# Optimization experiments

Measured on AMD Instinct MI355X. Metric: run time of the kernel, lower is better.

The kernel has to match this reference:

```python
import jax, jax.numpy as jnp
import numpy as np
from jax import lax

B, T, I, H, O = 256, 128, 512, 1024, 512


def setup_inputs() -> dict:
    key = jax.random.key(0)
    ks = jax.random.split(key, 7)
    s = 1.0 / np.sqrt(H)  # PyTorch LSTM/Linear init bound
    x = jax.random.normal(ks[0], (B, T, I), dtype=jnp.float32)
    W_ih = jax.random.uniform(ks[1], (4 * H, I), jnp.float32, -s, s)
    W_hh = jax.random.uniform(ks[2], (4 * H, H), jnp.float32, -s, s)
    b_ih = jax.random.uniform(ks[3], (4 * H,), jnp.float32, -s, s)
    b_hh = jax.random.uniform(ks[4], (4 * H,), jnp.float32, -s, s)
    W_fc = jax.random.uniform(ks[5], (O, H), jnp.float32, -s, s)
    b_fc = jax.random.uniform(ks[6], (O,), jnp.float32, -s, s)
    return {"x": x, "W_ih": W_ih, "W_hh": W_hh, "b_ih": b_ih,
            "b_hh": b_hh, "W_fc": W_fc, "b_fc": b_fc}


def _lstm_last(x, W_ih, W_hh, b_ih, b_hh):
    # Precompute input contribution for all timesteps: [T, B, 4H]
    pre = jnp.einsum('bti,gi->tbg', x, W_ih) + b_ih + b_hh

    def step(carry, xg):
        h, c = carry
        gates = xg + h @ W_hh.T  # [B, 4H]
        i, f, g, o = jnp.split(gates, 4, axis=-1)  # PyTorch gate order i,f,g,o
        c = jax.nn.sigmoid(f) * c + jax.nn.sigmoid(i) * jnp.tanh(g)
        h = jax.nn.sigmoid(o) * jnp.tanh(c)
        return (h, c), None

    h0 = jnp.zeros((x.shape[0], W_hh.shape[1]), x.dtype)
    (h, c), _ = lax.scan(step, (h0, h0), pre)
    return h, c


def reference(x, W_ih, W_hh, b_ih, b_hh, W_fc, b_fc):
    h, c = _lstm_last(x, W_ih, W_hh, b_ih, b_hh)
    out = h @ W_fc.T + b_fc  # fc on last timestep hidden
    # hidden returned as (h_n, c_n) with leading n_layers=1 dim, as in PyTorch
    return out, (h[None], c[None])
```

## Files before the change

kernel.cpp:

```cpp
#include <hip/hip_runtime.h>

typedef short bf8 __attribute__((ext_vector_type(8)));
typedef float f32x4 __attribute__((ext_vector_type(4)));
typedef uint u32x4 __attribute__((ext_vector_type(4)));

static constexpr int BB = 256;
static constexpr int TT = 128;
static constexpr int II = 512;
static constexpr int HH = 1024;
static constexpr int OO = 512;
static constexpr int G4 = 4096;

static constexpr size_t OUT_H = (size_t)BB * OO;
static constexpr size_t OUT_C = OUT_H + (size_t)BB * HH;
static constexpr size_t HBUF  = (size_t)BB * HH;

__device__ __forceinline__ float bf2f(ushort u) {
    unsigned v = ((unsigned)u) << 16;
    return __builtin_bit_cast(float, v);
}
__device__ __forceinline__ ushort f2bf(float f) {
    unsigned x = __builtin_bit_cast(unsigned, f);
    x = x + 0x7FFFu + ((x >> 16) & 1u);
    return (ushort)(x >> 16);
}
__device__ __forceinline__ float sigf(float x) { return 1.0f / (1.0f + __expf(-x)); }
__device__ __forceinline__ float tanhf_(float x) { return 2.0f * sigf(2.0f * x) - 1.0f; }

__device__ __forceinline__ void st_wt_short(const ushort* p, uint v) {
    asm volatile("global_store_short %0, %1, off sc0 sc1" :: "v"(p), "v"(v) : "memory");
}
__device__ __forceinline__ void st_wt_b64(const ushort* p, uint2 v) {
    asm volatile("global_store_dwordx2 %0, %1, off sc0 sc1" :: "v"(p), "v"(v) : "memory");
}
__device__ __forceinline__ void ld_bp_ushort_issue(uint& dst, const ushort* p) {
    asm volatile("global_load_ushort %0, %1, off sc0 sc1" : "=v"(dst) : "v"(p) : "memory");
}
__device__ __forceinline__ void ld_bp_b128_issue(u32x4& dst, const ushort* p) {
    asm volatile("global_load_dwordx4 %0, %1, off sc0 sc1" : "=v"(dst) : "v"(p) : "memory");
}
__device__ __forceinline__ void ld_c_b128_issue(u32x4& dst, const ushort* p) {
    asm volatile("global_load_dwordx4 %0, %1, off" : "=v"(dst) : "v"(p) : "memory");
}
__device__ __forceinline__ void wait_vm0() {
    asm volatile("s_waitcnt vmcnt(0)" ::: "memory");
    __builtin_amdgcn_sched_barrier(0);
}
#define WAITVM(N) do { asm volatile("s_waitcnt vmcnt(" #N ")" ::: "memory"); \
                       __builtin_amdgcn_sched_barrier(0); } while (0)

__device__ __forceinline__ void lightbar(int* slots, int bg, int gen) {
    asm volatile("s_waitcnt vmcnt(0) lgkmcnt(0)" ::: "memory");
    __builtin_amdgcn_sched_barrier(0);
    __syncthreads();
    int tid = threadIdx.x;
    if (tid == 0)
        asm volatile("global_store_dword %0, %1, off sc0 sc1" :: "v"(slots + bg * 32), "v"(gen) : "memory");
    if (tid < 64) {
        const int* sp = slots + tid * 32;
        int v;
        do {
            asm volatile("global_load_dword %0, %1, off sc0 sc1\n\ts_waitcnt vmcnt(0)"
                         : "=v"(v) : "v"(sp) : "memory");
            if (v >= gen) break;
            __builtin_amdgcn_s_sleep(1);
        } while (true);
    }
    __syncthreads();
}

__global__ void k_init(int* flags) {
    int i = blockIdx.x * 256 + threadIdx.x;
    if (i < 8192) flags[i] = 0;
}

__global__ void k_cast(const float* __restrict__ src, ushort* __restrict__ dst, int n4) {
    int i = blockIdx.x * blockDim.x + threadIdx.x;
    int stride = gridDim.x * blockDim.x;
    for (; i < n4; i += stride) {
        float4 v = ((const float4*)src)[i];
        ushort4 o;
        o.x = f2bf(v.x); o.y = f2bf(v.y); o.z = f2bf(v.z); o.w = f2bf(v.w);
        ((ushort4*)dst)[i] = o;
    }
}

__global__ void k_prep_w(const float* __restrict__ w, ushort* __restrict__ wp,
                         const float* __restrict__ bi, const float* __restrict__ bh,
                         float* __restrict__ bp, int Kdim) {
    int p = blockIdx.x;
    int orig = ((p >> 4) & 3) * HH + ((p >> 6) << 4) + (p & 15);
    const float* src = w + (size_t)orig * Kdim;
    ushort* dst = wp + (size_t)p * Kdim;
    for (int k = threadIdx.x; k < Kdim; k += 256) dst[k] = f2bf(src[k]);
    if (threadIdx.x == 0 && bp) bp[p] = bi[orig] + bh[orig];
}

template <int HMODE>
__global__ __launch_bounds__(256) void k_main(
    const float* __restrict__ x, const ushort* __restrict__ wpih,
    const float* __restrict__ bp, ushort* __restrict__ pre,
    const ushort* __restrict__ wphh, ushort* __restrict__ hbf,
    float* __restrict__ dout, int* flags, int SEG) {
    __shared__ ushort wl[32 * 2048];
    __shared__ ushort Al[64 * 32];
    __shared__ ushort Bl[128 * 32];

    int tid = threadIdx.x;
    int bid = blockIdx.x;
    int g = bid >> 6, j = bid & 63;
    int row0 = g << 6;
    int* slots = flags + g * 2048;
    int gen = 0;
    int nseg = TT / SEG;

    int w = tid >> 6, l = tid & 63;
    int l15 = l & 15, kg = l >> 4;
    int wbase = ((l15 << 6) + (kg << 4)) ^ ((l15 & 7) << 4);

    {
        const ushort* wsrc = wphh + (size_t)(j << 6) * HH;
        for (int s = 0; s < 32; ++s) {
            int cidx = (s << 8) + tid;
            int c = cidx >> 7;
            int kc = cidx & 127;
            uint4 v = *(const uint4*)(wsrc + (size_t)c * HH + (kc << 3));
            int byte = ((kc >> 2) << 12) + ((((c << 6) + ((kc & 3) << 4))) ^ ((c & 7) << 4));
            *(uint4*)((char*)wl + byte) = v;
        }
        int r = tid >> 2, hc = (tid & 3) << 2;
        uint2 z; z.x = 0; z.y = 0;
        st_wt_b64(hbf + (size_t)(row0 + r) * HH + (j << 4) + hc, z);
    }

    int wm = w >> 1, wn = w & 1;
    int r0 = tid >> 2, kk = tid & 3;
    int sbyteA = ((r0 << 6) + (kk << 4)) ^ ((r0 & 7) << 4);
    int sbyteB1 = sbyteA + 4096;

    const ushort* hbase = hbf + (size_t)(row0 + (w << 4) + l15) * HH + (kg << 3);
    int drow = row0 + (w << 4) + (kg << 2);
    int hcol = (j << 4) + l15;
    ushort* hobase = hbf + (size_t)drow * HH + hcol;
    const ushort* pbase = pre + (size_t)drow * G4 + (j << 6) + l15;
    float creg[4] = {0.f, 0.f, 0.f, 0.f};

    for (int sg = 0; sg < nseg; ++sg) {
        int t0 = sg * SEG;
        int ntiles = SEG << 5;
        for (int q = j; q < ntiles; q += 64) {
            int trel = q >> 5;
            int t = t0 + trel;
            int n0 = (q & 31) << 7;
            const float* xa = x + ((size_t)(row0 + r0) * TT + t) * II + (kk << 3);
            const ushort* gb0 = wpih + (size_t)(n0 + r0) * II + (kk << 3);
            const ushort* gb1 = gb0 + (size_t)64 * II;
            f32x4 acc[2][4];
#pragma unroll
            for (int mi = 0; mi < 2; ++mi)
#pragma unroll
                for (int ni = 0; ni < 4; ++ni) acc[mi][ni] = f32x4{0.f, 0.f, 0.f, 0.f};
            float4 a0 = *(const float4*)xa;
            float4 a1 = *(const float4*)(xa + 4);
            uint4 b0v = *(const uint4*)gb0;
            uint4 b1v = *(const uint4*)gb1;
            for (int ko = 0; ko < 16; ++ko) {
                union { ushort us[8]; uint4 v; } pa;
                pa.us[0] = f2bf(a0.x); pa.us[1] = f2bf(a0.y); pa.us[2] = f2bf(a0.z); pa.us[3] = f2bf(a0.w);
                pa.us[4] = f2bf(a1.x); pa.us[5] = f2bf(a1.y); pa.us[6] = f2bf(a1.z); pa.us[7] = f2bf(a1.w);
                __syncthreads();
                *(uint4*)((char*)Al + sbyteA) = pa.v;
                *(uint4*)((char*)Bl + sbyteA) = b0v;
                *(uint4*)((char*)Bl + sbyteB1) = b1v;
                __syncthreads();
                if (ko < 15) {
                    int k = (ko + 1) << 5;
                    a0 = *(const float4*)(xa + k);
                    a1 = *(const float4*)(xa + k + 4);
                    b0v = *(const uint4*)(gb0 + k);
                    b1v = *(const uint4*)(gb1 + k);
                }
                bf8 af[2], bv[4];
#pragma unroll
                for (int mi = 0; mi < 2; ++mi)
                    af[mi] = *(const bf8*)((char*)Al + wm * 2048 + mi * 1024 + wbase);
#pragma unroll
                for (int ni = 0; ni < 4; ++ni)
                    bv[ni] = *(const bf8*)((char*)Bl + wn * 4096 + ni * 1024 + wbase);
#pragma unroll
                for (int mi = 0; mi < 2; ++mi)
#pragma unroll
                    for (int ni = 0; ni < 4; ++ni)
                        acc[mi][ni] = __builtin_amdgcn_mfma_f32_16x16x32_bf16(af[mi], bv[ni], acc[mi][ni], 0, 0, 0);
            }
#pragma unroll
            for (int ni = 0; ni < 4; ++ni) {
                int col = n0 + wn * 64 + ni * 16 + l15;
                float bias = bp[col];
#pragma unroll
                for (int mi = 0; mi < 2; ++mi) {
                    int arow = row0 + wm * 32 + mi * 16 + (kg << 2);
#pragma unroll
                    for (int r = 0; r < 4; ++r)
                        st_wt_short(pre + ((size_t)trel * BB + arow + r) * G4 + col,
                                    (uint)f2bf(acc[mi][ni][r] + bias));
                }
            }
        }
        gen++; lightbar(slots, j, gen);

        uint prn[16];
#pragma unroll
        for (int ni = 0; ni < 4; ++ni)
#pragma unroll
            for (int r = 0; r < 4; ++r)
                ld_bp_ushort_issue(prn[ni * 4 + r], pbase + (size_t)r * G4 + (ni << 4));
        wait_vm0();

        for (int trel = 0; trel < SEG; ++trel) {
            int t = t0 + trel;
            int rb = HMODE ? (t & 1) : t;
            int wb = HMODE ? ((t & 1) ^ 1) : (t + 1);
            const ushort* hr = hbase + (size_t)rb * HBUF;
            u32x4 xv[8], yv[8];

#define ISSUE8(B, C) \
            _Pragma("unroll") \
            for (int u = 0; u < 8; ++u) { \
                if constexpr (HMODE == 0) ld_c_b128_issue(B[u], hr + (((C) * 8 + u) << 5)); \
                else ld_bp_b128_issue(B[u], hr + (((C) * 8 + u) << 5)); \
            }
#define CONSUME8(B, C) \
            _Pragma("unroll") \
            for (int u = 0; u < 8; ++u) { \
                int ko = (C) * 8 + u; \
                bf8 a = __builtin_bit_cast(bf8, B[u]); \
                _Pragma("unroll") \
                for (int ni = 0; ni < 4; ++ni) { \
                    bf8 b = *(const bf8*)((char*)wl + ko * 4096 + ni * 1024 + wbase); \
                    acc[ni] = __builtin_amdgcn_mfma_f32_16x16x32_bf16(a, b, acc[ni], 0, 0, 0); \
                } \
            }

            f32x4 acc[4];
            ISSUE8(xv, 0)
            ISSUE8(yv, 1)
#pragma unroll
            for (int ni = 0; ni < 4; ++ni)
#pragma unroll
                for (int r = 0; r < 4; ++r) acc[ni][r] = bf2f((ushort)prn[ni * 4 + r]);
            WAITVM(8);
            CONSUME8(xv, 0)
            ISSUE8(xv, 2)
            WAITVM(8);
            CONSUME8(yv, 1)
            ISSUE8(yv, 3)
            WAITVM(8);
            CONSUME8(xv, 2)
            {
                int nrel = (trel + 1 < SEG) ? trel + 1 : 0;
                const ushort* pnn = pre + ((size_t)nrel * BB + drow) * G4 + (j << 6) + l15;
#pragma unroll
                for (int ni = 0; ni < 4; ++ni)
#pragma unroll
                    for (int r = 0; r < 4; ++r)
                        ld_bp_ushort_issue(prn[ni * 4 + r], pnn + (size_t)r * G4 + (ni << 4));
            }
            WAITVM(16);
            CONSUME8(yv, 3)
#undef ISSUE8
#undef CONSUME8

            ushort* ho = hobase + (size_t)wb * HBUF;
            bool last = (t == TT - 1);
#pragma unroll
            for (int r = 0; r < 4; ++r) {
                float ig = sigf(acc[0][r]);
                float fg = sigf(acc[1][r]);
                float gg = tanhf_(acc[2][r]);
                float og = sigf(acc[3][r]);
                float c = fg * creg[r] + ig * gg;
                creg[r] = c;
                float h = og * tanhf_(c);
                st_wt_short(ho + (size_t)r * HH, (uint)f2bf(h));
                if (last) {
                    dout[OUT_H + (size_t)(drow + r) * HH + hcol] = h;
                    dout[OUT_C + (size_t)(drow + r) * HH + hcol] = c;
                }
            }
            gen++; lightbar(slots, j, gen);
        }
    }
}

__global__ __launch_bounds__(256) void k_fc(const ushort* __restrict__ hlast,
                                            const ushort* __restrict__ wfc,
                                            const float* __restrict__ bfc,
                                            float* __restrict__ out) {
    int tid = threadIdx.x;
    int b0 = (blockIdx.x >> 3) << 6;
    int n0 = (blockIdx.x & 7) << 6;
    int w = tid >> 6, l = tid & 63;
    int l15 = l & 15, kg = l >> 4;
    const ushort* ha = hlast + (size_t)(b0 + (w << 4) + l15) * HH + (kg << 3);
    f32x4 acc[4];
#pragma unroll
    for (int ni = 0; ni < 4; ++ni) acc[ni] = f32x4{0.f, 0.f, 0.f, 0.f};
    for (int ko = 0; ko < 32; ++ko) {
        bf8 a = *(const bf8*)(ha + (ko << 5));
#pragma unroll
        for (int ni = 0; ni < 4; ++ni) {
            bf8 b = *(const bf8*)(wfc + (size_t)(n0 + ni * 16 + l15) * HH + (ko << 5) + (kg << 3));
            acc[ni] = __builtin_amdgcn_mfma_f32_16x16x32_bf16(a, b, acc[ni], 0, 0, 0);
        }
    }
    int drow = b0 + (w << 4) + (kg << 2);
#pragma unroll
    for (int ni = 0; ni < 4; ++ni) {
        int col = n0 + ni * 16 + l15;
        float bias = bfc[col];
#pragma unroll
        for (int r = 0; r < 4; ++r)
            out[(size_t)(drow + r) * OO + col] = acc[ni][r] + bias;
    }
}

extern "C" void kernel_launch(void* const* d_in, const int* in_sizes, int n_in,
                              void* d_out, int out_size, void* d_ws, size_t ws_size,
                              hipStream_t stream) {
    const float* x   = (const float*)d_in[0];
    const float* Wih = (const float*)d_in[1];
    const float* Whh = (const float*)d_in[2];
    const float* bih = (const float*)d_in[3];
    const float* bhh = (const float*)d_in[4];
    const float* Wfc = (const float*)d_in[5];
    const float* bfc = (const float*)d_in[6];
    float* out = (float*)d_out;

    char* ws = (char*)d_ws;
    size_t off = 0;
    ushort* wpih = (ushort*)(ws + off); off += (size_t)G4 * II * 2;
    ushort* wphh = (ushort*)(ws + off); off += (size_t)G4 * HH * 2;
    ushort* wfcb = (ushort*)(ws + off); off += (size_t)OO * HH * 2;
    float*  bp   = (float*)(ws + off);  off += (size_t)G4 * 4;
    int*    flags= (int*)(ws + off);    off += 8192 * 4;
    size_t fixed = off;
    size_t HB2 = (size_t)BB * HH * 2;

    int HMODE = 0, SEG = 16;
    size_t hsz = (size_t)(TT + 1) * HB2;
    while (SEG > 1 && fixed + hsz + (size_t)SEG * BB * G4 * 2 > ws_size) SEG >>= 1;
    if (fixed + hsz + (size_t)SEG * BB * G4 * 2 > ws_size) {
        HMODE = 1; SEG = 16; hsz = 2 * HB2;
        while (SEG > 1 && fixed + hsz + (size_t)SEG * BB * G4 * 2 > ws_size) SEG >>= 1;
    }
    ushort* hbf = (ushort*)(ws + fixed);
    ushort* pre = (ushort*)(ws + fixed + hsz);
    const ushort* hlast = HMODE ? hbf : (hbf + (size_t)TT * HBUF);

    k_init<<<32, 256, 0, stream>>>(flags);
    k_cast<<<256, 256, 0, stream>>>(Wfc, wfcb, OO * HH / 4);
    k_prep_w<<<G4, 256, 0, stream>>>(Wih, wpih, bih, bhh, bp, II);
    k_prep_w<<<G4, 256, 0, stream>>>(Whh, wphh, nullptr, nullptr, nullptr, HH);
    if (HMODE == 0)
        k_main<0><<<256, 256, 0, stream>>>(x, wpih, bp, pre, wphh, hbf, out, flags, SEG);
    else
        k_main<1><<<256, 256, 0, stream>>>(x, wpih, bp, pre, wphh, hbf, out, flags, SEG);
    k_fc<<<32, 256, 0, stream>>>(hlast, wfcb, bfc, out);
}
```

Baseline: 1.515 ms.

## Use double-buffered h only and issue all h loads upfront per step

Removes the full per-timestep h history mode and always uses a two-buffer ping-pong h stored with cache-bypassing loads. Within each recurrent step, all 32 h-vector loads are issued at once into four register banks, plus the next step's preactivation prefetch, before any MFMA runs. This is meant to expose more memory-level parallelism and shorten the per-step latency chain. It costs more VGPRs, and h reads now always bypass cache where the previous default path may have used cached loads.

```diff
diff --git a/kernel.cpp b/kernel.cpp
--- a/kernel.cpp
+++ b/kernel.cpp
@@ -38,9 +38,6 @@
 }
 __device__ __forceinline__ void ld_bp_b128_issue(u32x4& dst, const ushort* p) {
     asm volatile("global_load_dwordx4 %0, %1, off sc0 sc1" : "=v"(dst) : "v"(p) : "memory");
-}
-__device__ __forceinline__ void ld_c_b128_issue(u32x4& dst, const ushort* p) {
-    asm volatile("global_load_dwordx4 %0, %1, off" : "=v"(dst) : "v"(p) : "memory");
 }
 __device__ __forceinline__ void wait_vm0() {
     asm volatile("s_waitcnt vmcnt(0)" ::: "memory");
@@ -96,7 +93,6 @@
     if (threadIdx.x == 0 && bp) bp[p] = bi[orig] + bh[orig];
 }
 
-template <int HMODE>
 __global__ __launch_bounds__(256) void k_main(
     const float* __restrict__ x, const ushort* __restrict__ wpih,
     const float* __restrict__ bp, ushort* __restrict__ pre,
@@ -219,17 +215,12 @@
 
         for (int trel = 0; trel < SEG; ++trel) {
             int t = t0 + trel;
-            int rb = HMODE ? (t & 1) : t;
-            int wb = HMODE ? ((t & 1) ^ 1) : (t + 1);
-            const ushort* hr = hbase + (size_t)rb * HBUF;
-            u32x4 xv[8], yv[8];
+            const ushort* hr = hbase + (size_t)(t & 1) * HBUF;
+            u32x4 xv[8], yv[8], zv[8], wv[8];
 
 #define ISSUE8(B, C) \
             _Pragma("unroll") \
-            for (int u = 0; u < 8; ++u) { \
-                if constexpr (HMODE == 0) ld_c_b128_issue(B[u], hr + (((C) * 8 + u) << 5)); \
-                else ld_bp_b128_issue(B[u], hr + (((C) * 8 + u) << 5)); \
-            }
+            for (int u = 0; u < 8; ++u) ld_bp_b128_issue(B[u], hr + (((C) * 8 + u) << 5));
 #define CONSUME8(B, C) \
             _Pragma("unroll") \
             for (int u = 0; u < 8; ++u) { \
@@ -245,33 +236,36 @@
             f32x4 acc[4];
             ISSUE8(xv, 0)
             ISSUE8(yv, 1)
-#pragma unroll
-            for (int ni = 0; ni < 4; ++ni)
-#pragma unroll
-                for (int r = 0; r < 4; ++r) acc[ni][r] = bf2f((ushort)prn[ni * 4 + r]);
-            WAITVM(8);
-            CONSUME8(xv, 0)
-            ISSUE8(xv, 2)
-            WAITVM(8);
-            CONSUME8(yv, 1)
-            ISSUE8(yv, 3)
-            WAITVM(8);
-            CONSUME8(xv, 2)
+            ISSUE8(zv, 2)
+            ISSUE8(wv, 3)
             {
                 int nrel = (trel + 1 < SEG) ? trel + 1 : 0;
                 const ushort* pnn = pre + ((size_t)nrel * BB + drow) * G4 + (j << 6) + l15;
+                uint tmp[16];
 #pragma unroll
                 for (int ni = 0; ni < 4; ++ni)
 #pragma unroll
                     for (int r = 0; r < 4; ++r)
-                        ld_bp_ushort_issue(prn[ni * 4 + r], pnn + (size_t)r * G4 + (ni << 4));
-            }
+                        ld_bp_ushort_issue(tmp[ni * 4 + r], pnn + (size_t)r * G4 + (ni << 4));
+#pragma unroll
+                for (int ni = 0; ni < 4; ++ni)
+#pragma unroll
+                    for (int r = 0; r < 4; ++r) acc[ni][r] = bf2f((ushort)prn[ni * 4 + r]);
+#pragma unroll
+                for (int q2 = 0; q2 < 16; ++q2) prn[q2] = tmp[q2];
+            }
+            WAITVM(40);
+            CONSUME8(xv, 0)
+            WAITVM(32);
+            CONSUME8(yv, 1)
+            WAITVM(24);
+            CONSUME8(zv, 2)
             WAITVM(16);
-            CONSUME8(yv, 3)
+            CONSUME8(wv, 3)
 #undef ISSUE8
 #undef CONSUME8
 
-            ushort* ho = hobase + (size_t)wb * HBUF;
+            ushort* ho = hobase + (size_t)((t & 1) ^ 1) * HBUF;
             bool last = (t == TT - 1);
 #pragma unroll
             for (int r = 0; r < 4; ++r) {
@@ -344,27 +338,16 @@
     ushort* wfcb = (ushort*)(ws + off); off += (size_t)OO * HH * 2;
     float*  bp   = (float*)(ws + off);  off += (size_t)G4 * 4;
     int*    flags= (int*)(ws + off);    off += 8192 * 4;
+    ushort* hbf  = (ushort*)(ws + off); off += (size_t)2 * BB * HH * 2;
     size_t fixed = off;
-    size_t HB2 = (size_t)BB * HH * 2;
-
-    int HMODE = 0, SEG = 16;
-    size_t hsz = (size_t)(TT + 1) * HB2;
-    while (SEG > 1 && fixed + hsz + (size_t)SEG * BB * G4 * 2 > ws_size) SEG >>= 1;
-    if (fixed + hsz + (size_t)SEG * BB * G4 * 2 > ws_size) {
-        HMODE = 1; SEG = 16; hsz = 2 * HB2;
-        while (SEG > 1 && fixed + hsz + (size_t)SEG * BB * G4 * 2 > ws_size) SEG >>= 1;
-    }
-    ushort* hbf = (ushort*)(ws + fixed);
-    ushort* pre = (ushort*)(ws + fixed + hsz);
-    const ushort* hlast = HMODE ? hbf : (hbf + (size_t)TT * HBUF);
+    int SEG = 16;
+    while (SEG > 1 && fixed + (size_t)SEG * BB * G4 * 2 > ws_size) SEG >>= 1;
+    ushort* pre = (ushort*)(ws + fixed);
 
     k_init<<<32, 256, 0, stream>>>(flags);
     k_cast<<<256, 256, 0, stream>>>(Wfc, wfcb, OO * HH / 4);
     k_prep_w<<<G4, 256, 0, stream>>>(Wih, wpih, bih, bhh, bp, II);
     k_prep_w<<<G4, 256, 0, stream>>>(Whh, wphh, nullptr, nullptr, nullptr, HH);
-    if (HMODE == 0)
-        k_main<0><<<256, 256, 0, stream>>>(x, wpih, bp, pre, wphh, hbf, out, flags, SEG);
-    else
-        k_main<1><<<256, 256, 0, stream>>>(x, wpih, bp, pre, wphh, hbf, out, flags, SEG);
-    k_fc<<<32, 256, 0, stream>>>(hlast, wfcb, bfc, out);
-}
+    k_main<<<256, 256, 0, stream>>>(x, wpih, bp, pre, wphh, hbf, out, flags, SEG);
+    k_fc<<<32, 256, 0, stream>>>(hbf, wfcb, bfc, out);
+}
```

Measured after the change: 1.759 ms. 1.16x slower.
